# Performance work log

Measured on AMD Instinct MI355X. Metric: run time of the kernel, lower is better.

Reference implementation:

```python
import jax, jax.numpy as jnp
import numpy as np

NEG = -1e30  # log-domain 'zero' (safe stand-in for -inf)


def _ctc_loss(logits, labels, label_length, logit_length):
    """Dense-label CTC loss, blank = last class, logits [B,T,C] batch-major.

    Matches tf.nn.ctc_loss(blank_index=-1, logits_time_major=False):
    per-example negative log-likelihood via the standard forward algorithm
    on the blank-extended label sequence of length S = 2L+1.
    """
    B, T, C = logits.shape
    L = labels.shape[1]
    S = 2 * L + 1
    blank = C - 1

    logp = jax.nn.log_softmax(logits, axis=-1)           # [B,T,C]
    lp_t = jnp.moveaxis(logp, 1, 0)                      # [T,B,C]

    # Extended label: blank, l1, blank, l2, ..., blank
    y_ext = jnp.full((B, S), blank, dtype=labels.dtype).at[:, 1::2].set(labels)
    s_idx = jnp.arange(S)
    # s -> s-2 skip allowed iff current symbol is a non-blank differing from s-2
    y_m2 = jnp.pad(y_ext, ((0, 0), (2, 0)), constant_values=blank)[:, :-2]
    skip = (s_idx[None, :] >= 2) & (y_ext != blank) & (y_ext != y_m2)  # [B,S]

    emit0 = jnp.take_along_axis(lp_t[0], y_ext, axis=1)  # [B,S]
    alpha0 = jnp.where(s_idx[None, :] <= 1, emit0, NEG)  # paths start at s=0 or 1

    def step(alpha, lp):
        emit = jnp.take_along_axis(lp, y_ext, axis=1)                      # [B,S]
        a1 = jnp.pad(alpha, ((0, 0), (1, 0)), constant_values=NEG)[:, :-1]  # s-1
        a2 = jnp.pad(alpha, ((0, 0), (2, 0)), constant_values=NEG)[:, :-2]  # s-2
        a2 = jnp.where(skip, a2, NEG)
        new = jnp.logaddexp(jnp.logaddexp(alpha, a1), a2) + emit
        return new, new

    _, alphas = jax.lax.scan(step, alpha0, lp_t[1:])     # [T-1,B,S]
    alphas = jnp.concatenate([alpha0[None], alphas], axis=0)  # [T,B,S]

    b = jnp.arange(B)
    final = alphas[logit_length - 1, b]                  # [B,S] alpha at last frame
    end = 2 * label_length                               # index of final blank
    nll = -jnp.logaddexp(final[b, end], final[b, end - 1])
    return jnp.mean(nll)


def setup_inputs() -> dict:
    key = jax.random.key(0)
    k1, k2, k3 = jax.random.split(key, 3)
    B, T, C, L = 256, 256, 512, 64
    logits = jax.random.normal(k1, (B, T, C), dtype=jnp.float32)
    labels = jax.random.randint(k2, (B, L), 0, C - 1, dtype=jnp.int32)  # never blank
    label_length = jax.random.randint(k3, (B,), 16, L + 1, dtype=jnp.int32)
    logit_length = jnp.full((B,), T, dtype=jnp.int32)
    return {"logits": logits, "labels": labels,
            "label_length": label_length, "logit_length": logit_length}


def reference(logits, labels, label_length, logit_length):
    return _ctc_loss(logits, labels, label_length, logit_length)
```

## Files before the change

kernel.cpp:

```cpp
#include <hip/hip_runtime.h>
#include <math.h>

#define NEGV -1e30f

constexpr int Bc = 256;
constexpr int Tc = 256;
constexpr int Cc = 512;
constexpr int Lc = 64;
constexpr int PW = 8;
constexpr int NGRP = Tc / PW;
constexpr int EMS = 65;
constexpr float INVLN2 = 1.44269504088896340736f;
constexpr float LN2    = 0.69314718055994530942f;

__device__ __forceinline__ float la2(float a, float b) {
    float m = fmaxf(a, b);
    float d = fabsf(a - b);
    return m + __log2f(exp2f(-d) + 1.0f);
}

__device__ __forceinline__ float dpp_shr1(float x, float fill) {
    int r = __builtin_amdgcn_update_dpp(__float_as_int(fill), __float_as_int(x),
                                        0x138 , 0xF, 0xF, false);
    return __int_as_float(r);
}

__global__ __launch_bounds__(576) void ctc_k(const float* __restrict__ logits,
                                             const int* __restrict__ labels,
                                             const int* __restrict__ lab_len,
                                             const int* __restrict__ log_len,
                                             float* __restrict__ nll) {
    const int b    = blockIdx.x;
    const int tid  = threadIdx.x;
    const int w    = tid >> 6;
    const int lane = tid & 63;

    __shared__ float rows[PW][Cc];
    __shared__ float em[Tc * EMS];
    __shared__ int   cnt[NGRP];

    if (tid < NGRP) cnt[tid] = 0;
    __syncthreads();

    const float* base = logits + (size_t)b * Tc * Cc;
    const int y = labels[b * Lc + lane];

    if (w < PW) {
        float* myrow = rows[w];
        const float4* p0 = (const float4*)(base + (size_t)w * Cc);
        float4 c0 = p0[lane], c1 = p0[lane + 64];
        for (int i = 0; i < NGRP; ++i) {
            const int t = w + PW * i;
            float4 n0, n1;
            if (i + 1 < NGRP) {
                const float4* pn = (const float4*)(base + (size_t)(t + PW) * Cc);
                n0 = pn[lane]; n1 = pn[lane + 64];
            }
            ((float4*)myrow)[lane]      = c0;
            ((float4*)myrow)[lane + 64] = c1;
            float e = __expf(c0.x) + __expf(c0.y) + __expf(c0.z) + __expf(c0.w)
                    + __expf(c1.x) + __expf(c1.y) + __expf(c1.z) + __expf(c1.w);
#pragma unroll
            for (int o = 32; o; o >>= 1) e += __shfl_xor(e, o, 64);
            float lse2 = __log2f(e);
            float xl = myrow[y];
            em[t * EMS + lane] = xl * INVLN2 - lse2;
            if (lane == 63)
                em[t * EMS + 64] = c1.w * INVLN2 - lse2;
            __hip_atomic_fetch_add(&cnt[i], 1, __ATOMIC_RELEASE,
                                   __HIP_MEMORY_SCOPE_WORKGROUP);
            c0 = n0; c1 = n1;
        }
    } else {
        const int  prevlab = __shfl_up(y, 1, 64);
        const bool skip    = (lane >= 1) && (y != prevlab);
        const int  llm1    = log_len[b] - 1;
        float ae = NEGV, ao = NEGV, ax = NEGV;
        float fe = NEGV, fo = NEGV, fx = NEGV;

        auto step = [&](float em_lv, float em_bv, int t) {
            float q  = la2(ao, ae);
            float x2 = la2(ax, ao);
            float po = dpp_shr1(ao, NEGV);
            float nae = la2(ae, po) + em_bv;
            float nao = (skip ? la2(q, po) : q) + em_lv;
            float nax = x2 + em_bv;
            ae = nae; ao = nao; ax = nax;
            if (t == llm1) { fe = ae; fo = ao; fx = ax; }
        };

        for (int g = 0; g < NGRP; ++g) {
            while (__hip_atomic_load(&cnt[g], __ATOMIC_ACQUIRE,
                                     __HIP_MEMORY_SCOPE_WORKGROUP) < PW)
                __builtin_amdgcn_s_sleep(1);
            float el[PW], eb[PW];
#pragma unroll
            for (int r = 0; r < PW; ++r) {
                el[r] = em[(PW * g + r) * EMS + lane];
                eb[r] = em[(PW * g + r) * EMS + 64];
            }
            if (g == 0) {
                ae = (lane == 0) ? eb[0] : NEGV;
                ao = (lane == 0) ? el[0] : NEGV;
                ax = NEGV;
                if (llm1 == 0) { fe = ae; fo = ao; fx = ax; }
#pragma unroll
                for (int r = 1; r < PW; ++r) step(el[r], eb[r], r);
            } else {
#pragma unroll
                for (int r = 0; r < PW; ++r) step(el[r], eb[r], PW * g + r);
            }
        }

        const int L  = lab_len[b];
        float f0 = (L == Lc) ? __shfl(fx, 63, 64) : __shfl(fe, L, 64);
        float f1 = __shfl(fo, L - 1, 64);
        if (lane == 0) nll[b] = -LN2 * la2(f0, f1);
    }
}

__global__ __launch_bounds__(256) void reduce_k(const float* __restrict__ nll,
                                                float* __restrict__ out) {
    int tid = threadIdx.x;
    float v = nll[tid];
#pragma unroll
    for (int o = 32; o; o >>= 1) v += __shfl_xor(v, o, 64);
    __shared__ float pr[4];
    if ((tid & 63) == 0) pr[tid >> 6] = v;
    __syncthreads();
    if (tid == 0) out[0] = (pr[0] + pr[1] + pr[2] + pr[3]) * (1.0f / Bc);
}

extern "C" void kernel_launch(void* const* d_in, const int* in_sizes, int n_in,
                              void* d_out, int out_size, void* d_ws, size_t ws_size,
                              hipStream_t stream) {
    const float* logits  = (const float*)d_in[0];
    const int*   labels  = (const int*)d_in[1];
    const int*   lab_len = (const int*)d_in[2];
    const int*   log_len = (const int*)d_in[3];
    float* out = (float*)d_out;
    float* nll = (float*)d_ws;

    hipLaunchKernelGGL(ctc_k, dim3(Bc), dim3(576), 0, stream,
                       logits, labels, lab_len, log_len, nll);
    hipLaunchKernelGGL(reduce_k, dim3(1), dim3(256), 0, stream, nll, out);
}
```

Baseline: 198.9 us.

## Replace atomic-counter handoff with lockstep barrier phases and double-buffered emissions

Swaps the spin-wait atomic counters and the full-sequence emission buffer for a phase loop. Each phase has producer waves compute one time step apiece and the consumer wave process the previous group, synchronised by a workgroup barrier over a small double-buffered shared array. It also gathers the label logits straight from global memory instead of staging rows in LDS, uses a DPP-based wave reduction in place of shuffles, and uses a three-way log-sum-exp for the skip path. The barriers tie producer progress to the consumer's step time, which could serialise work the old design overlapped freely.

Result: no change. 201.6 us (+1.4%).

```diff
diff --git a/kernel.cpp b/kernel.cpp
--- a/kernel.cpp
+++ b/kernel.cpp
@@ -8,8 +8,7 @@
 constexpr int Cc = 512;
 constexpr int Lc = 64;
 constexpr int PW = 8;
-constexpr int NGRP = Tc / PW;
-constexpr int EMS = 65;
+constexpr int NPH = Tc / PW;
 constexpr float INVLN2 = 1.44269504088896340736f;
 constexpr float LN2    = 0.69314718055994530942f;
 
@@ -19,10 +18,37 @@
     return m + __log2f(exp2f(-d) + 1.0f);
 }
 
+__device__ __forceinline__ float lse3(float a, float b, float c) {
+    float m = fmaxf(fmaxf(a, b), c);
+    return m + __log2f(exp2f(a - m) + exp2f(b - m) + exp2f(c - m));
+}
+
 __device__ __forceinline__ float dpp_shr1(float x, float fill) {
     int r = __builtin_amdgcn_update_dpp(__float_as_int(fill), __float_as_int(x),
                                         0x138 , 0xF, 0xF, false);
     return __int_as_float(r);
+}
+
+__device__ __forceinline__ float wave_sum_dpp(float v) {
+#define DPPADD(ctrl)                                                          \
+    v += __int_as_float(__builtin_amdgcn_update_dpp(                          \
+        0, __float_as_int(v), (ctrl), 0xF, 0xF, true))
+    DPPADD(0x111);
+    DPPADD(0x112);
+    DPPADD(0x114);
+    DPPADD(0x118);
+    DPPADD(0x142);
+    DPPADD(0x143);
+#undef DPPADD
+    return __int_as_float(__builtin_amdgcn_readlane(__float_as_int(v), 63));
+}
+
+__device__ __forceinline__ void phase_barrier() {
+    __builtin_amdgcn_sched_barrier(0);
+    asm volatile("s_waitcnt lgkmcnt(0)" ::: "memory");
+    __builtin_amdgcn_sched_barrier(0);
+    __builtin_amdgcn_s_barrier();
+    __builtin_amdgcn_sched_barrier(0);
 }
 
 __global__ __launch_bounds__(576) void ctc_k(const float* __restrict__ logits,
@@ -35,83 +61,78 @@
     const int w    = tid >> 6;
     const int lane = tid & 63;
 
-    __shared__ float rows[PW][Cc];
-    __shared__ float em[Tc * EMS];
-    __shared__ int   cnt[NGRP];
-
-    if (tid < NGRP) cnt[tid] = 0;
-    __syncthreads();
+    __shared__ float em[2][PW][66];
 
     const float* base = logits + (size_t)b * Tc * Cc;
     const int y = labels[b * Lc + lane];
 
+    float4 c0, c1; float cg;
     if (w < PW) {
-        float* myrow = rows[w];
         const float4* p0 = (const float4*)(base + (size_t)w * Cc);
-        float4 c0 = p0[lane], c1 = p0[lane + 64];
-        for (int i = 0; i < NGRP; ++i) {
-            const int t = w + PW * i;
-            float4 n0, n1;
-            if (i + 1 < NGRP) {
-                const float4* pn = (const float4*)(base + (size_t)(t + PW) * Cc);
-                n0 = pn[lane]; n1 = pn[lane + 64];
+        c0 = p0[lane]; c1 = p0[lane + 64];
+        cg = base[(size_t)w * Cc + y];
+    }
+
+    const int  prevlab = __shfl_up(y, 1, 64);
+    const bool skip    = (lane >= 1) && (y != prevlab);
+    const int  llm1    = log_len[b] - 1;
+    float ae = NEGV, ao = NEGV, ax = NEGV;
+    float fe = NEGV, fo = NEGV, fx = NEGV;
+
+    auto step = [&](float em_lv, float em_bv, int t) {
+        float po = dpp_shr1(ao, NEGV);
+        float nae = la2(ae, po) + em_bv;
+        float nao = (skip ? lse3(ao, ae, po)
+                          : la2(ao, ae)) + em_lv;
+        float nax = la2(ax, ao) + em_bv;
+        ae = nae; ao = nao; ax = nax;
+        if (t == llm1) { fe = ae; fo = ao; fx = ax; }
+    };
+
+    auto consume = [&](int g) {
+        const float (*rd)[66] = em[g & 1];
+        float el[PW], eb[PW];
+#pragma unroll
+        for (int r = 0; r < PW; ++r) { el[r] = rd[r][lane]; eb[r] = rd[r][64]; }
+        const int t0 = g * PW;
+        if (g == 0) {
+            ae = (lane == 0) ? eb[0] : NEGV;
+            ao = (lane == 0) ? el[0] : NEGV;
+            ax = NEGV;
+            if (llm1 == 0) { fe = ae; fo = ao; fx = ax; }
+#pragma unroll
+            for (int r = 1; r < PW; ++r) step(el[r], eb[r], r);
+        } else {
+#pragma unroll
+            for (int r = 0; r < PW; ++r) step(el[r], eb[r], t0 + r);
+        }
+    };
+
+    for (int p = 0; p < NPH; ++p) {
+        if (w < PW) {
+            const int t = p * PW + w;
+            float4 n0, n1; float ng;
+            if (p + 1 < NPH) {
+                const float4* q =
+                    (const float4*)(base + (size_t)(t + PW) * Cc);
+                n0 = q[lane]; n1 = q[lane + 64];
+                ng = base[(size_t)(t + PW) * Cc + y];
             }
-            ((float4*)myrow)[lane]      = c0;
-            ((float4*)myrow)[lane + 64] = c1;
             float e = __expf(c0.x) + __expf(c0.y) + __expf(c0.z) + __expf(c0.w)
                     + __expf(c1.x) + __expf(c1.y) + __expf(c1.z) + __expf(c1.w);
-#pragma unroll
-            for (int o = 32; o; o >>= 1) e += __shfl_xor(e, o, 64);
-            float lse2 = __log2f(e);
-            float xl = myrow[y];
-            em[t * EMS + lane] = xl * INVLN2 - lse2;
+            float lse2 = __log2f(wave_sum_dpp(e));
+            em[p & 1][w][lane] = cg * INVLN2 - lse2;
             if (lane == 63)
-                em[t * EMS + 64] = c1.w * INVLN2 - lse2;
-            __hip_atomic_fetch_add(&cnt[i], 1, __ATOMIC_RELEASE,
-                                   __HIP_MEMORY_SCOPE_WORKGROUP);
-            c0 = n0; c1 = n1;
+                em[p & 1][w][64] = c1.w * INVLN2 - lse2;
+            c0 = n0; c1 = n1; cg = ng;
+        } else if (p > 0) {
+            consume(p - 1);
         }
-    } else {
-        const int  prevlab = __shfl_up(y, 1, 64);
-        const bool skip    = (lane >= 1) && (y != prevlab);
-        const int  llm1    = log_len[b] - 1;
-        float ae = NEGV, ao = NEGV, ax = NEGV;
-        float fe = NEGV, fo = NEGV, fx = NEGV;
+        phase_barrier();
+    }
 
-        auto step = [&](float em_lv, float em_bv, int t) {
-            float q  = la2(ao, ae);
-            float x2 = la2(ax, ao);
-            float po = dpp_shr1(ao, NEGV);
-            float nae = la2(ae, po) + em_bv;
-            float nao = (skip ? la2(q, po) : q) + em_lv;
-            float nax = x2 + em_bv;
-            ae = nae; ao = nao; ax = nax;
-            if (t == llm1) { fe = ae; fo = ao; fx = ax; }
-        };
-
-        for (int g = 0; g < NGRP; ++g) {
-            while (__hip_atomic_load(&cnt[g], __ATOMIC_ACQUIRE,
-                                     __HIP_MEMORY_SCOPE_WORKGROUP) < PW)
-                __builtin_amdgcn_s_sleep(1);
-            float el[PW], eb[PW];
-#pragma unroll
-            for (int r = 0; r < PW; ++r) {
-                el[r] = em[(PW * g + r) * EMS + lane];
-                eb[r] = em[(PW * g + r) * EMS + 64];
-            }
-            if (g == 0) {
-                ae = (lane == 0) ? eb[0] : NEGV;
-                ao = (lane == 0) ? el[0] : NEGV;
-                ax = NEGV;
-                if (llm1 == 0) { fe = ae; fo = ao; fx = ax; }
-#pragma unroll
-                for (int r = 1; r < PW; ++r) step(el[r], eb[r], r);
-            } else {
-#pragma unroll
-                for (int r = 0; r < PW; ++r) step(el[r], eb[r], PW * g + r);
-            }
-        }
-
+    if (w == PW) {
+        consume(NPH - 1);
         const int L  = lab_len[b];
         float f0 = (L == Lc) ? __shfl(fx, 63, 64) : __shfl(fe, L, 64);
         float f1 = __shfl(fo, L - 1, 64);
```
